# Performance work log

Measured on AMD Instinct MI355X. Metric: run time of the kernel, lower is better.

## Reference

```python
import jax, jax.numpy as jnp
import numpy as np

B, C, U = 8, 32, 32
K = 5            # powers = k + 1 with k = 4
N1, N2 = 256, 256


def setup_inputs() -> dict:
    key = jax.random.key(0)
    k_x, k_c1, k_c2, k_w = jax.random.split(key, 4)
    x = jax.random.normal(k_x, (B, C, N1, N2), dtype=jnp.float32)
    # Chebyshev polynomial bases T_0..T_k of the (rescaled) Laplacians of the
    # two factor graphs; registered buffers in the torch module.
    cheb1 = jax.random.normal(k_c1, (K, N1, N1), dtype=jnp.float32)
    cheb2 = jax.random.normal(k_c2, (K, N2, N2), dtype=jnp.float32)
    # Trainable anisotropic coefficients [powers, powers, channels, units],
    # initialized N(0, 0.001) in the original module.
    coefs = jax.random.normal(k_w, (K, K, C, U), dtype=jnp.float32) * 0.001
    return {"x": x, "cheb1": cheb1, "cheb2": cheb2, "coefs": coefs}


def reference(x, cheb1, cheb2, coefs):
    """Fused form of the anisotropic Chebyshev convolution.

    Original triple loop computes
      out[b,u,m,n] = sum_{k1,k2,i,p,q}
          coefs[k1,k2,i,u] * cheb1[k1,p,m] * cheb2[k2,q,n] * x[b,i,p,q]
    """
    # Filter along the first graph axis for every power k1: [B, K, C, N1, N2]
    a = jnp.einsum('kpm,bipq->bkimq', cheb1, x)
    # Contract channels and k1 with the learned coefficients: [B, K, U, N1, N2]
    c = jnp.einsum('bkimq,kliu->blumq', a, coefs)
    # Filter along the second graph axis for every power k2: [B, U, N1, N2]
    out = jnp.einsum('blumq,lqn->bumn', c, cheb2)
    return out
```

## Files before the change

### kernel.cpp

```cpp
#include <hip/hip_runtime.h>
#include <stdint.h>

#define WB 8
#define WC 32
#define WU 32
#define WK 5
#define WN 256
#define NN 65536
#define KC 160
#define KQ 1280

typedef __attribute__((ext_vector_type(8))) short bf8;
typedef __attribute__((ext_vector_type(8))) unsigned short us8;
typedef __attribute__((ext_vector_type(4))) float f4;

__device__ __forceinline__ unsigned short f2b(float f) {
    union { float f; uint32_t u; } v; v.f = f;
    uint32_t u = v.u;
    return (unsigned short)((u + 0x7FFFu + ((u >> 16) & 1u)) >> 16);
}

__device__ __forceinline__ void gload16(const unsigned short* g, unsigned short* l) {
    __builtin_amdgcn_global_load_lds(
        (const __attribute__((address_space(1))) unsigned int*)g,
        (__attribute__((address_space(3))) unsigned int*)l, 16, 0, 0);
}

__global__ void prep_small(const float* __restrict__ cheb1,
                           const float* __restrict__ cheb2,
                           const float* __restrict__ coefs,
                           unsigned short* __restrict__ c1T,
                           unsigned short* __restrict__ c2T,
                           unsigned short* __restrict__ Wt) {
    int idx = blockIdx.x * 256 + threadIdx.x;
    if (idx < WK * NN) {
        int k = idx / NN, r = idx % NN, m = r / WN, p = r % WN;
        c1T[idx] = f2b(cheb1[(k * WN + p) * WN + m]);
    }
    if (idx < WN * KQ) {
        int n = idx / KQ, r = idx % KQ;
        c2T[idx] = f2b(cheb2[r * WN + n]);
    }
    if (idx < KC * KC) {
        int lu = idx / KC, ki = idx % KC;
        int l = lu >> 5, u = lu & 31, k = ki >> 5, i = ki & 31;
        Wt[idx] = f2b(coefs[((k * WK + l) * WC + i) * WU + u]);
    }
}

__global__ void prep_x(const float* __restrict__ x, unsigned short* __restrict__ xT) {
    __shared__ unsigned short tile[64][72];
    int bi = blockIdx.z;
    int p0 = blockIdx.y * 64, q0 = blockIdx.x * 64;
    const float* src = x + (size_t)bi * NN;
    unsigned short* dst = xT + (size_t)bi * NN;
    int t = threadIdx.x;
    int c4 = (t & 15) * 4, r0 = t >> 4;
    for (int it = 0; it < 4; ++it) {
        int r = r0 + it * 16;
        float4 v = *reinterpret_cast<const float4*>(&src[(size_t)(p0 + r) * WN + q0 + c4]);
        tile[r][c4 + 0] = f2b(v.x); tile[r][c4 + 1] = f2b(v.y);
        tile[r][c4 + 2] = f2b(v.z); tile[r][c4 + 3] = f2b(v.w);
    }
    __syncthreads();
    for (int it = 0; it < 4; ++it) {
        int q = r0 + it * 16;
        ushort4 o;
        o.x = tile[c4 + 0][q]; o.y = tile[c4 + 1][q];
        o.z = tile[c4 + 2][q]; o.w = tile[c4 + 3][q];
        *reinterpret_cast<ushort4*>(&dst[(size_t)(q0 + q) * WN + p0 + c4]) = o;
    }
}

__global__ __launch_bounds__(256, 3) void g1(const unsigned short* __restrict__ c1T,
                                             const unsigned short* __restrict__ xT,
                                             unsigned short* __restrict__ a, int b_base) {
    __shared__ unsigned short As[128 * 64];
    __shared__ unsigned short Bs[128 * 64];
    int z = blockIdx.z;
    int bl = z >> 5, i = z & 31;
    int row0 = blockIdx.y * 128;
    int q0 = blockIdx.x * 128;
    int b = b_base + bl;
    const unsigned short* Asrc = c1T;
    const unsigned short* Bsrc = xT + (size_t)(b * WC + i) * NN;
    unsigned short* Out = a + (size_t)bl * KC * NN;

    int t = threadIdx.x;
    int w = t >> 6, l = t & 63;
    int wm = (w & 1) * 64, wn = (w >> 1) * 64;
    int lr = l & 15, hi = l >> 4;
    int srow = l >> 3;
    int scol = ((l & 7) ^ srow) * 8;

    f4 acc[4][4];
    for (int mf = 0; mf < 4; ++mf) for (int nf = 0; nf < 4; ++nf) acc[mf][nf] = (f4)(0.0f);

    for (int p0 = 0; p0 < 256; p0 += 64) {
        __syncthreads();
        for (int it = 0; it < 4; ++it) {
            int chunk = it * 4 + w;
            int row = chunk * 8 + srow;
            gload16(&Asrc[(size_t)(row0 + row) * 256 + p0 + scol], &As[chunk * 512]);
            gload16(&Bsrc[(size_t)(q0 + row) * 256 + p0 + scol], &Bs[chunk * 512]);
        }
        __syncthreads();
        bf8 af[2][4], bfr[2][4];
        for (int kk = 0; kk < 2; ++kk)
            for (int mf = 0; mf < 4; ++mf) {
                int r = wm + mf * 16 + lr;
                af[kk][mf] = *(const bf8*)&As[r * 64 + (((kk * 4 + hi) ^ (r & 7)) * 8)];
                int rb = wn + mf * 16 + lr;
                bfr[kk][mf] = *(const bf8*)&Bs[rb * 64 + (((kk * 4 + hi) ^ (rb & 7)) * 8)];
            }
        for (int kk = 0; kk < 2; ++kk)
            for (int mf = 0; mf < 4; ++mf)
                for (int nf = 0; nf < 4; ++nf)
                    acc[mf][nf] = __builtin_amdgcn_mfma_f32_16x16x32_bf16(af[kk][mf], bfr[kk][nf], acc[mf][nf], 0, 0, 0);
    }
    for (int mf = 0; mf < 4; ++mf)
        for (int nf = 0; nf < 4; ++nf)
            for (int j = 0; j < 4; ++j) {
                int grow = row0 + wm + mf * 16 + hi * 4 + j;
                int k = grow >> 8, m = grow & 255;
                int q = q0 + wn + nf * 16 + lr;
                Out[(size_t)(k * 32 + i) * NN + m * 256 + q] = f2b(acc[mf][nf][j]);
            }
}

__global__ __launch_bounds__(512, 4) void g2p(const unsigned short* __restrict__ Wt,
                                              const unsigned short* __restrict__ a,
                                              unsigned short* __restrict__ c) {
    __shared__ unsigned short Bt[128 * 172];
    int bl = blockIdx.y;
    int n0 = blockIdx.x * 128;
    const unsigned short* asrc = a + (size_t)bl * KC * NN;
    unsigned short* Out = c + (size_t)bl * KC * NN;
    int t = threadIdx.x;

    for (int s = 0; s < 5; ++s) {
        int id = t + s * 512;
        int oct = id & 15, ki = id >> 4;
        us8 v = *(const us8*)&asrc[(size_t)ki * NN + n0 + oct * 8];
        #pragma unroll
        for (int j = 0; j < 8; ++j)
            Bt[(oct * 8 + j) * 172 + ki] = v[j];
    }
    __syncthreads();

    int w = t >> 6, l = t & 63;
    int mh = w >> 2, nq = w & 3;
    int lr = l & 15, hi = l >> 4;
    f4 acc[5][2];
    for (int mf = 0; mf < 5; ++mf) { acc[mf][0] = (f4)(0.0f); acc[mf][1] = (f4)(0.0f); }

    for (int kk = 0; kk < 5; ++kk) {
        int k0 = kk * 32 + hi * 8;
        bf8 bfr[2];
        #pragma unroll
        for (int nf = 0; nf < 2; ++nf) {
            int pix = (nq * 2 + nf) * 16 + lr;
            typedef __attribute__((ext_vector_type(4))) short s4v;
            s4v lo  = *(const s4v*)&Bt[pix * 172 + k0];
            s4v hi4 = *(const s4v*)&Bt[pix * 172 + k0 + 4];
            bfr[nf] = __builtin_shufflevector(lo, hi4, 0, 1, 2, 3, 4, 5, 6, 7);
        }
        #pragma unroll
        for (int mf = 0; mf < 5; ++mf) {
            int row = mh * 80 + mf * 16 + lr;
            bf8 afr = *(const bf8*)&Wt[(size_t)row * KC + k0];
            acc[mf][0] = __builtin_amdgcn_mfma_f32_16x16x32_bf16(afr, bfr[0], acc[mf][0], 0, 0, 0);
            acc[mf][1] = __builtin_amdgcn_mfma_f32_16x16x32_bf16(afr, bfr[1], acc[mf][1], 0, 0, 0);
        }
    }
    for (int mf = 0; mf < 5; ++mf)
        for (int nf = 0; nf < 2; ++nf)
            for (int j = 0; j < 4; ++j) {
                int row = mh * 80 + mf * 16 + hi * 4 + j;
                int col = n0 + (nq * 2 + nf) * 16 + lr;
                Out[(size_t)row * NN + col] = f2b(acc[mf][nf][j]);
            }
}

__global__ __launch_bounds__(512, 4) void g3(const unsigned short* __restrict__ c,
                                             const unsigned short* __restrict__ c2T,
                                             float* __restrict__ out, int b_base) {
    __shared__ unsigned short As[128 * 64];
    __shared__ unsigned short Bs[256 * 64];
    int bl = blockIdx.y;
    int b = b_base + bl;
    int R0 = blockIdx.x * 128;
    int u = R0 >> 8, m0 = R0 & 255;
    const unsigned short* Csrc = c + (size_t)bl * KC * NN;

    int t = threadIdx.x;
    int w = t >> 6, l = t & 63;
    int wm = (w >> 2) * 64, wn = (w & 3) * 64;
    int lr = l & 15, hi = l >> 4;
    int srow = l >> 3;
    int scol = ((l & 7) ^ srow) * 8;

    f4 acc[4][4];
    for (int mf = 0; mf < 4; ++mf) for (int nf = 0; nf < 4; ++nf) acc[mf][nf] = (f4)(0.0f);

    for (int step = 0; step < 20; ++step) {
        int lq = step >> 2, q0 = (step & 3) * 64;
        const unsigned short* Arow0 = Csrc + (size_t)(lq * 32 + u) * NN + (size_t)m0 * 256 + q0;
        const unsigned short* Brow0 = c2T + step * 64;
        __syncthreads();
        for (int it = 0; it < 2; ++it) {
            int chunk = it * 8 + w;
            int row = chunk * 8 + srow;
            gload16(&Arow0[(size_t)row * 256 + scol], &As[chunk * 512]);
        }
        for (int it = 0; it < 4; ++it) {
            int chunk = it * 8 + w;
            int row = chunk * 8 + srow;
            gload16(&Brow0[(size_t)row * KQ + scol], &Bs[chunk * 512]);
        }
        __syncthreads();
        for (int kk = 0; kk < 2; ++kk) {
            bf8 af[4], bfr[4];
            for (int mf = 0; mf < 4; ++mf) {
                int r = wm + mf * 16 + lr;
                af[mf] = *(const bf8*)&As[r * 64 + (((kk * 4 + hi) ^ (r & 7)) * 8)];
            }
            for (int nf = 0; nf < 4; ++nf) {
                int rb = wn + nf * 16 + lr;
                bfr[nf] = *(const bf8*)&Bs[rb * 64 + (((kk * 4 + hi) ^ (rb & 7)) * 8)];
            }
            for (int mf = 0; mf < 4; ++mf)
                for (int nf = 0; nf < 4; ++nf)
                    acc[mf][nf] = __builtin_amdgcn_mfma_f32_16x16x32_bf16(af[mf], bfr[nf], acc[mf][nf], 0, 0, 0);
        }
    }
    for (int mf = 0; mf < 4; ++mf)
        for (int nf = 0; nf < 4; ++nf)
            for (int j = 0; j < 4; ++j) {
                int m = m0 + wm + mf * 16 + hi * 4 + j;
                int n = wn + nf * 16 + lr;
                out[((size_t)(b * WU + u) * WN + m) * WN + n] = acc[mf][nf][j];
            }
}

extern "C" void kernel_launch(void* const* d_in, const int* in_sizes, int n_in,
                              void* d_out, int out_size, void* d_ws, size_t ws_size,
                              hipStream_t stream) {
    const float* x     = (const float*)d_in[0];
    const float* cheb1 = (const float*)d_in[1];
    const float* cheb2 = (const float*)d_in[2];
    const float* coefs = (const float*)d_in[3];
    float* out = (float*)d_out;
    unsigned short* ws = (unsigned short*)d_ws;

    size_t off = 0;
    unsigned short* xT  = ws + off; off += (size_t)WB * WC * NN;
    unsigned short* c1T = ws + off; off += (size_t)WK * NN;
    unsigned short* c2T = ws + off; off += (size_t)WN * KQ;
    unsigned short* Wt  = ws + off; off += (size_t)KC * KC;
    size_t fixed_elems = off;
    size_t a1 = (size_t)KC * NN;

    prep_small<<<1280, 256, 0, stream>>>(cheb1, cheb2, coefs, c1T, c2T, Wt);
    prep_x<<<dim3(4, 4, WB * WC), 256, 0, stream>>>(x, xT);

    size_t avail = ws_size / 2;
    size_t rem = avail > fixed_elems ? avail - fixed_elems : 0;

    if (rem >= 9 * a1) {
        int nb = (int)((rem - 8 * a1) / a1);
        if (nb < 1) nb = 1;
        if (nb > WB) nb = WB;
        unsigned short* a_ = ws + fixed_elems;
        unsigned short* c_ = a_ + (size_t)nb * a1;
        for (int b0 = 0; b0 < WB; b0 += nb) {
            int cur = (WB - b0 < nb) ? (WB - b0) : nb;
            g1<<<dim3(2, 10, cur * 32), 256, 0, stream>>>(c1T, xT, a_, b0);
            g2p<<<dim3(512, cur), 512, 0, stream>>>(Wt, a_, c_ + (size_t)b0 * a1);
        }
        g3<<<dim3(64, WB), 512, 0, stream>>>(c_, c2T, out, 0);
    } else {
        size_t per_b = 2 * a1;
        int nb = (int)(rem / per_b);
        if (nb < 1) nb = 1;
        if (nb > WB) nb = WB;
        unsigned short* a_ = ws + fixed_elems;
        unsigned short* c_ = a_ + (size_t)nb * a1;
        for (int b0 = 0; b0 < WB; b0 += nb) {
            int cur = (WB - b0 < nb) ? (WB - b0) : nb;
            g1<<<dim3(2, 10, cur * 32), 256, 0, stream>>>(c1T, xT, a_, b0);
            g2p<<<dim3(512, cur), 512, 0, stream>>>(Wt, a_, c_);
            g3<<<dim3(64, cur), 512, 0, stream>>>(c_, c2T, out, b0);
        }
    }
}
```

Baseline: 278.4 us.

## Double-buffer g3 LDS loads and widen g2p transpose stores

The g3 GEMM now prefetches the next K-step into a second LDS buffer with global_load_lds while computing on the current one. It replaces the two __syncthreads per step with s_waitcnt vmcnt plus raw barriers, and lowers the launch bound occupancy from 4 to 2 to fit the doubled shared memory. Separately, the g2p transpose loads four k-rows per thread and writes ushort4 packed stores into LDS instead of scalar 2-byte stores. The aim is to hide global load latency and cut LDS store count, at the cost of fewer resident blocks. The hand-tuned vmcnt count is fragile and must match the number of loads in flight.

```diff
diff --git a/kernel.cpp b/kernel.cpp
--- a/kernel.cpp
+++ b/kernel.cpp
@@ -138,13 +138,22 @@
     unsigned short* Out = c + (size_t)bl * KC * NN;
     int t = threadIdx.x;
 
-    for (int s = 0; s < 5; ++s) {
-        int id = t + s * 512;
-        int oct = id & 15, ki = id >> 4;
-        us8 v = *(const us8*)&asrc[(size_t)ki * NN + n0 + oct * 8];
-        #pragma unroll
-        for (int j = 0; j < 8; ++j)
-            Bt[(oct * 8 + j) * 172 + ki] = v[j];
+    for (int s = 0; s < 2; ++s) {
+        int task = t + s * 512;
+        if (task < 640) {
+            int oct = task & 15, kq = task >> 4;
+            const unsigned short* src = asrc + (size_t)(kq * 4) * NN + n0 + oct * 8;
+            us8 v0 = *(const us8*)&src[0 * NN];
+            us8 v1 = *(const us8*)&src[1 * NN];
+            us8 v2 = *(const us8*)&src[2 * NN];
+            us8 v3 = *(const us8*)&src[3 * NN];
+            #pragma unroll
+            for (int j = 0; j < 8; ++j) {
+                ushort4 wv;
+                wv.x = v0[j]; wv.y = v1[j]; wv.z = v2[j]; wv.w = v3[j];
+                *reinterpret_cast<ushort4*>(&Bt[(oct * 8 + j) * 172 + kq * 4]) = wv;
+            }
+        }
     }
     __syncthreads();
 
@@ -182,11 +191,11 @@
             }
 }
 
-__global__ __launch_bounds__(512, 4) void g3(const unsigned short* __restrict__ c,
+__global__ __launch_bounds__(512, 2) void g3(const unsigned short* __restrict__ c,
                                              const unsigned short* __restrict__ c2T,
                                              float* __restrict__ out, int b_base) {
-    __shared__ unsigned short As[128 * 64];
-    __shared__ unsigned short Bs[256 * 64];
+    __shared__ unsigned short As[2][128 * 64];
+    __shared__ unsigned short Bs[2][256 * 64];
     int bl = blockIdx.y;
     int b = b_base + bl;
     int R0 = blockIdx.x * 128;
@@ -203,37 +212,47 @@
     f4 acc[4][4];
     for (int mf = 0; mf < 4; ++mf) for (int nf = 0; nf < 4; ++nf) acc[mf][nf] = (f4)(0.0f);
 
+#define G3_STAGE(buf, step) do { \
+    int lq_ = (step) >> 2, q0_ = ((step) & 3) * 64; \
+    const unsigned short* Arow0 = Csrc + (size_t)(lq_ * 32 + u) * NN + (size_t)m0 * 256 + q0_; \
+    const unsigned short* Brow0 = c2T + (step) * 64; \
+    for (int it = 0; it < 2; ++it) { \
+        int chunk = it * 8 + w; int row = chunk * 8 + srow; \
+        gload16(&Arow0[(size_t)row * 256 + scol], &As[buf][chunk * 512]); } \
+    for (int it = 0; it < 4; ++it) { \
+        int chunk = it * 8 + w; int row = chunk * 8 + srow; \
+        gload16(&Brow0[(size_t)row * KQ + scol], &Bs[buf][chunk * 512]); } \
+} while (0)
+
+    G3_STAGE(0, 0);
     for (int step = 0; step < 20; ++step) {
-        int lq = step >> 2, q0 = (step & 3) * 64;
-        const unsigned short* Arow0 = Csrc + (size_t)(lq * 32 + u) * NN + (size_t)m0 * 256 + q0;
-        const unsigned short* Brow0 = c2T + step * 64;
-        __syncthreads();
-        for (int it = 0; it < 2; ++it) {
-            int chunk = it * 8 + w;
-            int row = chunk * 8 + srow;
-            gload16(&Arow0[(size_t)row * 256 + scol], &As[chunk * 512]);
-        }
-        for (int it = 0; it < 4; ++it) {
-            int chunk = it * 8 + w;
-            int row = chunk * 8 + srow;
-            gload16(&Brow0[(size_t)row * KQ + scol], &Bs[chunk * 512]);
-        }
-        __syncthreads();
+        int cur = step & 1;
+        if (step < 19) {
+            G3_STAGE(cur ^ 1, step + 1);
+            asm volatile("s_waitcnt vmcnt(6)" ::: "memory");
+        } else {
+            asm volatile("s_waitcnt vmcnt(0)" ::: "memory");
+        }
+        __builtin_amdgcn_s_barrier();
+        asm volatile("" ::: "memory");
         for (int kk = 0; kk < 2; ++kk) {
             bf8 af[4], bfr[4];
             for (int mf = 0; mf < 4; ++mf) {
                 int r = wm + mf * 16 + lr;
-                af[mf] = *(const bf8*)&As[r * 64 + (((kk * 4 + hi) ^ (r & 7)) * 8)];
+                af[mf] = *(const bf8*)&As[cur][r * 64 + (((kk * 4 + hi) ^ (r & 7)) * 8)];
             }
             for (int nf = 0; nf < 4; ++nf) {
                 int rb = wn + nf * 16 + lr;
-                bfr[nf] = *(const bf8*)&Bs[rb * 64 + (((kk * 4 + hi) ^ (rb & 7)) * 8)];
+                bfr[nf] = *(const bf8*)&Bs[cur][rb * 64 + (((kk * 4 + hi) ^ (rb & 7)) * 8)];
             }
             for (int mf = 0; mf < 4; ++mf)
                 for (int nf = 0; nf < 4; ++nf)
                     acc[mf][nf] = __builtin_amdgcn_mfma_f32_16x16x32_bf16(af[mf], bfr[nf], acc[mf][nf], 0, 0, 0);
         }
-    }
+        asm volatile("" ::: "memory");
+        __builtin_amdgcn_s_barrier();
+    }
+#undef G3_STAGE
     for (int mf = 0; mf < 4; ++mf)
         for (int nf = 0; nf < 4; ++nf)
             for (int j = 0; j < 4; ++j) {
```

Result: slower. 301.6 us (+8.3%).

## Widen g1 tile to full 256 columns with 512 threads; vectorize g2p transpose

Applied to the files above, without the earlier changes.

The first GEMM kernel now uses 512-thread blocks that each compute a 128x256 output tile covering the full q dimension. Each c1 row tile is loaded once per block instead of twice, and the grid drops from three dimensions to two. LDS for the B tile doubles and fragment loads move inside the k-step loop to limit register pressure. Separately, the g2p staging transpose now reads four k-rows per thread and writes ushort4 into shared memory, replacing scalar 16-bit stores with fewer, wider LDS writes.

```diff
diff --git a/kernel.cpp b/kernel.cpp
--- a/kernel.cpp
+++ b/kernel.cpp
@@ -72,15 +72,14 @@
     }
 }
 
-__global__ __launch_bounds__(256, 3) void g1(const unsigned short* __restrict__ c1T,
+__global__ __launch_bounds__(512, 4) void g1(const unsigned short* __restrict__ c1T,
                                              const unsigned short* __restrict__ xT,
                                              unsigned short* __restrict__ a, int b_base) {
     __shared__ unsigned short As[128 * 64];
-    __shared__ unsigned short Bs[128 * 64];
-    int z = blockIdx.z;
+    __shared__ unsigned short Bs[256 * 64];
+    int z = blockIdx.y;
     int bl = z >> 5, i = z & 31;
-    int row0 = blockIdx.y * 128;
-    int q0 = blockIdx.x * 128;
+    int row0 = blockIdx.x * 128;
     int b = b_base + bl;
     const unsigned short* Asrc = c1T;
     const unsigned short* Bsrc = xT + (size_t)(b * WC + i) * NN;
@@ -88,7 +87,7 @@
 
     int t = threadIdx.x;
     int w = t >> 6, l = t & 63;
-    int wm = (w & 1) * 64, wn = (w >> 1) * 64;
+    int wm = (w >> 2) * 64, wn = (w & 3) * 64;
     int lr = l & 15, hi = l >> 4;
     int srow = l >> 3;
     int scol = ((l & 7) ^ srow) * 8;
@@ -98,32 +97,38 @@
 
     for (int p0 = 0; p0 < 256; p0 += 64) {
         __syncthreads();
-        for (int it = 0; it < 4; ++it) {
-            int chunk = it * 4 + w;
+        for (int it = 0; it < 2; ++it) {
+            int chunk = it * 8 + w;
             int row = chunk * 8 + srow;
             gload16(&Asrc[(size_t)(row0 + row) * 256 + p0 + scol], &As[chunk * 512]);
-            gload16(&Bsrc[(size_t)(q0 + row) * 256 + p0 + scol], &Bs[chunk * 512]);
+        }
+        for (int it = 0; it < 4; ++it) {
+            int chunk = it * 8 + w;
+            int row = chunk * 8 + srow;
+            gload16(&Bsrc[(size_t)row * 256 + p0 + scol], &Bs[chunk * 512]);
         }
         __syncthreads();
-        bf8 af[2][4], bfr[2][4];
-        for (int kk = 0; kk < 2; ++kk)
+        for (int kk = 0; kk < 2; ++kk) {
+            bf8 af[4], bfr[4];
             for (int mf = 0; mf < 4; ++mf) {
                 int r = wm + mf * 16 + lr;
-                af[kk][mf] = *(const bf8*)&As[r * 64 + (((kk * 4 + hi) ^ (r & 7)) * 8)];
-                int rb = wn + mf * 16 + lr;
-                bfr[kk][mf] = *(const bf8*)&Bs[rb * 64 + (((kk * 4 + hi) ^ (rb & 7)) * 8)];
-            }
-        for (int kk = 0; kk < 2; ++kk)
+                af[mf] = *(const bf8*)&As[r * 64 + (((kk * 4 + hi) ^ (r & 7)) * 8)];
+            }
+            for (int nf = 0; nf < 4; ++nf) {
+                int rb = wn + nf * 16 + lr;
+                bfr[nf] = *(const bf8*)&Bs[rb * 64 + (((kk * 4 + hi) ^ (rb & 7)) * 8)];
+            }
             for (int mf = 0; mf < 4; ++mf)
                 for (int nf = 0; nf < 4; ++nf)
-                    acc[mf][nf] = __builtin_amdgcn_mfma_f32_16x16x32_bf16(af[kk][mf], bfr[kk][nf], acc[mf][nf], 0, 0, 0);
+                    acc[mf][nf] = __builtin_amdgcn_mfma_f32_16x16x32_bf16(af[mf], bfr[nf], acc[mf][nf], 0, 0, 0);
+        }
     }
     for (int mf = 0; mf < 4; ++mf)
         for (int nf = 0; nf < 4; ++nf)
             for (int j = 0; j < 4; ++j) {
                 int grow = row0 + wm + mf * 16 + hi * 4 + j;
                 int k = grow >> 8, m = grow & 255;
-                int q = q0 + wn + nf * 16 + lr;
+                int q = wn + nf * 16 + lr;
                 Out[(size_t)(k * 32 + i) * NN + m * 256 + q] = f2b(acc[mf][nf][j]);
             }
 }
@@ -138,13 +143,22 @@
     unsigned short* Out = c + (size_t)bl * KC * NN;
     int t = threadIdx.x;
 
-    for (int s = 0; s < 5; ++s) {
-        int id = t + s * 512;
-        int oct = id & 15, ki = id >> 4;
-        us8 v = *(const us8*)&asrc[(size_t)ki * NN + n0 + oct * 8];
-        #pragma unroll
-        for (int j = 0; j < 8; ++j)
-            Bt[(oct * 8 + j) * 172 + ki] = v[j];
+    for (int s = 0; s < 2; ++s) {
+        int task = t + s * 512;
+        if (task < 640) {
+            int oct = task & 15, kq = task >> 4;
+            const unsigned short* src = asrc + (size_t)(kq * 4) * NN + n0 + oct * 8;
+            us8 v0 = *(const us8*)&src[0 * NN];
+            us8 v1 = *(const us8*)&src[1 * NN];
+            us8 v2 = *(const us8*)&src[2 * NN];
+            us8 v3 = *(const us8*)&src[3 * NN];
+            #pragma unroll
+            for (int j = 0; j < 8; ++j) {
+                ushort4 wv;
+                wv.x = v0[j]; wv.y = v1[j]; wv.z = v2[j]; wv.w = v3[j];
+                *reinterpret_cast<ushort4*>(&Bt[(oct * 8 + j) * 172 + kq * 4]) = wv;
+            }
+        }
     }
     __syncthreads();
 
@@ -275,7 +289,7 @@
         unsigned short* c_ = a_ + (size_t)nb * a1;
         for (int b0 = 0; b0 < WB; b0 += nb) {
             int cur = (WB - b0 < nb) ? (WB - b0) : nb;
-            g1<<<dim3(2, 10, cur * 32), 256, 0, stream>>>(c1T, xT, a_, b0);
+            g1<<<dim3(10, cur * 32), 512, 0, stream>>>(c1T, xT, a_, b0);
             g2p<<<dim3(512, cur), 512, 0, stream>>>(Wt, a_, c_ + (size_t)b0 * a1);
         }
         g3<<<dim3(64, WB), 512, 0, stream>>>(c_, c2T, out, 0);
@@ -288,7 +302,7 @@
         unsigned short* c_ = a_ + (size_t)nb * a1;
         for (int b0 = 0; b0 < WB; b0 += nb) {
             int cur = (WB - b0 < nb) ? (WB - b0) : nb;
-            g1<<<dim3(2, 10, cur * 32), 256, 0, stream>>>(c1T, xT, a_, b0);
+            g1<<<dim3(10, cur * 32), 512, 0, stream>>>(c1T, xT, a_, b0);
             g2p<<<dim3(512, cur), 512, 0, stream>>>(Wt, a_, c_);
             g3<<<dim3(64, cur), 512, 0, stream>>>(c_, c2T, out, b0);
         }
```

Result: no change. 283.7 us (+1.9%).
